# Kernel optimization log

Hardware: AMD Instinct MI355X
Metric: run time of the kernel (lower is better)

## Reference

```python
import jax, jax.numpy as jnp
import numpy as np

V, D, H, L, FF, NA, NB, S, C, BS = 32000, 768, 12, 6, 3072, 2, 2, 512, 10, 16
MOE_LAYERS = (1, 3, 5)
NE = NA * NB


def _ln(x, g, b, eps=1e-5):
    m = x.mean(-1, keepdims=True)
    v = ((x - m) ** 2).mean(-1, keepdims=True)
    return (x - m) / jnp.sqrt(v + eps) * g + b


def _ffn(x, W1, B1, W2, B2):
    # GLU-style FFN: w2(a * silu(b)) where [a, b] = chunk(w1(x), 2)
    h = x @ W1.T + B1
    a, b = jnp.split(h, 2, -1)
    return (a * jax.nn.silu(b)) @ W2.T + B2


def _mha(x, wqkv, bqkv, wo, bo):
    Bq, Sq, d = x.shape
    dh = d // H
    qkv = x @ wqkv.T + bqkv
    q, k, v = jnp.split(qkv, 3, -1)
    q = q.reshape(Bq, Sq, H, dh).transpose(0, 2, 1, 3)
    k = k.reshape(Bq, Sq, H, dh).transpose(0, 2, 1, 3)
    v = v.reshape(Bq, Sq, H, dh).transpose(0, 2, 1, 3)
    scores = jnp.einsum('bhqd,bhkd->bhqk', q, k) / jnp.sqrt(jnp.float32(dh))
    attn = jax.nn.softmax(scores, axis=-1)
    o = jnp.einsum('bhqk,bhkd->bhqd', attn, v)
    o = o.transpose(0, 2, 1, 3).reshape(Bq, Sq, d)
    return o @ wo.T + bo


def _moe(xf, W1, B1, W2, B2, gAw, gAb, gBw, gBb):
    pA = jax.nn.softmax(xf @ gAw.T + gAb, axis=-1)  # [T, NA]
    pB = jax.nn.softmax(xf @ gBw.T + gBb, axis=-1)  # [T, NB]
    iA = jnp.argmax(pA, -1)
    iB = jnp.argmax(pB, -1)
    auxA = NA * (pA.mean(0) * jax.nn.one_hot(iA, NA).mean(0)).sum()
    auxB = NB * (pB.mean(0) * jax.nn.one_hot(iB, NB).mean(0)).sum()
    e = iA * NB + iB  # [T] flattened expert id
    # dense all-expert compute then per-token select (E is small = 4)
    h = jnp.einsum('td,efd->etf', xf, W1) + B1[:, None, :]  # [NE, T, 2*FF]
    a, b = jnp.split(h, 2, -1)
    y = jnp.einsum('etf,edf->etd', a * jax.nn.silu(b), W2) + B2[:, None, :]
    out = y[e, jnp.arange(xf.shape[0])]  # [T, D]
    return out, auxA + auxB


def _forward(tok_emb, pos_emb, wqkv, bqkv, wo, bo, ln1g, ln1b, ln2g, ln2b,
             dW1, dB1, dW2, dB2, mW1, mB1, mW2, mB2, gAw, gAb, gBw, gBb,
             cW1, cB1, cW2, cB2, input_ids):
    x = tok_emb[input_ids] + pos_emb[None, :, :]
    total_aux = jnp.float32(0.0)
    di = mi = 0
    for l in range(L):
        x = _ln(x + _mha(x, wqkv[l], bqkv[l], wo[l], bo[l]), ln1g[l], ln1b[l])
        if l in MOE_LAYERS:
            xf = x.reshape(BS * S, D)
            f, aux = _moe(xf, mW1[mi], mB1[mi], mW2[mi], mB2[mi],
                          gAw[mi], gAb[mi], gBw[mi], gBb[mi])
            mi += 1
            total_aux = total_aux + aux
            f = f.reshape(BS, S, D)
        else:
            f = _ffn(x, dW1[di], dB1[di], dW2[di], dB2[di])
            di += 1
        x = _ln(x + f, ln2g[l], ln2b[l])
    rep = x.mean(1)  # mean pooling (no cls token / mask)
    hcls = jax.nn.relu(rep @ cW1.T + cB1)
    logits = hcls @ cW2.T + cB2
    return logits, total_aux


def setup_inputs() -> dict:
    key = jax.random.key(0)
    ks = iter(jax.random.split(key, 48))
    r = lambda shape, s=0.02: jax.random.normal(next(ks), shape, jnp.float32) * s
    Ld, Lm = L - len(MOE_LAYERS), len(MOE_LAYERS)
    return dict(
        input_ids=jax.random.randint(next(ks), (BS, S), 0, V),
        tok_emb=r((V, D)),
        pos_emb=r((S, D), 0.01),
        wqkv=r((L, 3 * D, D)), bqkv=jnp.zeros((L, 3 * D), jnp.float32),
        wo=r((L, D, D)), bo=jnp.zeros((L, D), jnp.float32),
        ln1g=jnp.ones((L, D), jnp.float32), ln1b=jnp.zeros((L, D), jnp.float32),
        ln2g=jnp.ones((L, D), jnp.float32), ln2b=jnp.zeros((L, D), jnp.float32),
        dW1=r((Ld, 2 * FF, D)), dB1=jnp.zeros((Ld, 2 * FF), jnp.float32),
        dW2=r((Ld, D, FF)), dB2=jnp.zeros((Ld, D), jnp.float32),
        mW1=r((Lm, NE, 2 * FF, D)), mB1=jnp.zeros((Lm, NE, 2 * FF), jnp.float32),
        mW2=r((Lm, NE, D, FF)), mB2=jnp.zeros((Lm, NE, D), jnp.float32),
        gAw=r((Lm, NA, D)), gAb=jnp.zeros((Lm, NA), jnp.float32),
        gBw=r((Lm, NB, D)), gBb=jnp.zeros((Lm, NB), jnp.float32),
        cW1=r((D, D)), cB1=jnp.zeros((D,), jnp.float32),
        cW2=r((C, D)), cB2=jnp.zeros((C,), jnp.float32),
    )


def reference(input_ids, tok_emb, pos_emb, wqkv, bqkv, wo, bo, ln1g, ln1b,
              ln2g, ln2b, dW1, dB1, dW2, dB2, mW1, mB1, mW2, mB2,
              gAw, gAb, gBw, gBb, cW1, cB1, cW2, cB2):
    return _forward(tok_emb, pos_emb, wqkv, bqkv, wo, bo, ln1g, ln1b, ln2g,
                    ln2b, dW1, dB1, dW2, dB2, mW1, mB1, mW2, mB2,
                    gAw, gAb, gBw, gBb, cW1, cB1, cW2, cB2, input_ids)
```

## Files before the change

### kernel.cpp

```cpp
#include <hip/hip_runtime.h>
#include <cstddef>

#define TOK   8192
#define DIMD  768
#define NH    12
#define DHD   64
#define SEQ   512
#define NB_   16
#define FFD   3072
#define NEXP  4
#define CCLS  10
#define FF2   (2*FFD)

typedef short bf16x8 __attribute__((ext_vector_type(8)));
typedef float f32x4  __attribute__((ext_vector_type(4)));

static const size_t OFF_X    = 0;
static const size_t OFF_XB   = OFF_X   + (size_t)TOK*DIMD;
static const size_t OFF_F    = OFF_XB  + (size_t)TOK*DIMD/2;
static const size_t OFF_SH   = OFF_F   + (size_t)TOK*DIMD;
static const size_t SH_FL    = (size_t)8704*FF2/2;
static const size_t OFF_WQ   = OFF_SH  + SH_FL;
static const size_t OFF_WOB  = OFF_WQ  + (size_t)3*DIMD*DIMD/2;
static const size_t OFF_W1B  = OFF_WOB + (size_t)DIMD*DIMD/2;
static const size_t OFF_W2B  = OFF_W1B + (size_t)NEXP*FF2*DIMD/2;
static const size_t OFF_REP  = OFF_W2B + (size_t)NEXP*DIMD*FFD/2;
static const size_t OFF_HCLS = OFF_REP + (size_t)NB_*DIMD;
static const size_t OFF_STAT = OFF_HCLS+ (size_t)NB_*DIMD;
static const size_t OFF_INT  = OFF_STAT+ 8;
static const size_t OFF_AUX  = OFF_INT + 160;
static const size_t OFF_EID  = OFF_AUX + 1;
static const size_t OFF_PERM = OFF_EID + TOK;

__device__ __forceinline__ ushort f2bf(float f) {
    union { float f; unsigned u; } v; v.f = f;
    unsigned r = v.u + 0x7FFF + ((v.u >> 16) & 1);
    return (ushort)(r >> 16);
}
__device__ __forceinline__ float bf2f(ushort u) {
    union { unsigned u; float f; } v; v.u = ((unsigned)u) << 16;
    return v.f;
}
__device__ __forceinline__ void gload16(const void* g, void* l) {
    __builtin_amdgcn_global_load_lds((const __attribute__((address_space(1))) void*)g,
                                     (__attribute__((address_space(3))) void*)l, 16, 0, 0);
}

__device__ __forceinline__ void xcd_swizzle_cm(int& bx, int& by)
{
    int gx = gridDim.x, gy = gridDim.y;
    int bid = blockIdx.x * gy + blockIdx.y;
    int nwg = gx * gy;
    int q = nwg >> 3, r8 = nwg & 7;
    int xcd = bid & 7, loc = bid >> 3;
    int lbid = (xcd < r8 ? xcd * (q + 1) : r8 * (q + 1) + (xcd - r8) * q) + loc;
    bx = lbid / gy;
    by = lbid % gy;
}

__global__ __launch_bounds__(256) void k_cvt(const float* __restrict__ s, ushort* __restrict__ d, int n8)
{
    int i = blockIdx.x * 256 + threadIdx.x;
    if (i >= n8) return;
    float4 x0 = ((const float4*)s)[i * 2];
    float4 x1 = ((const float4*)s)[i * 2 + 1];
    ushort r[8] = { f2bf(x0.x), f2bf(x0.y), f2bf(x0.z), f2bf(x0.w),
                    f2bf(x1.x), f2bf(x1.y), f2bf(x1.z), f2bf(x1.w) };
    ((uint4*)d)[i] = *(uint4*)r;
}

__global__ __launch_bounds__(256) void k_embed(const int* __restrict__ ids,
                                               const float* __restrict__ te,
                                               const float* __restrict__ pe,
                                               float* __restrict__ x,
                                               ushort* __restrict__ xb)
{
    int i = blockIdx.x * 256 + threadIdx.x;
    const int nd4 = DIMD / 4;
    if (i >= TOK * nd4) return;
    int t = i / nd4, d4 = i % nd4;
    int s = t % SEQ;
    int id = ids[t];
    float4 a = ((const float4*)(te + (size_t)id * DIMD))[d4];
    float4 b = ((const float4*)(pe + (size_t)s  * DIMD))[d4];
    float4 o; o.x = a.x + b.x; o.y = a.y + b.y; o.z = a.z + b.z; o.w = a.w + b.w;
    ((float4*)(x + (size_t)t * DIMD))[d4] = o;
    ushort4 ob = make_ushort4(f2bf(o.x), f2bf(o.y), f2bf(o.z), f2bf(o.w));
    *(ushort4*)(xb + (size_t)t * DIMD + d4 * 4) = ob;
}

template<int GATHER, int SCAT>
__global__ __launch_bounds__(256) void k_mm(const ushort* __restrict__ A,
                                            const ushort* __restrict__ Wb,
                                            const float* __restrict__ bias,
                                            ushort* __restrict__ C_,
                                            int N, int K, int lda,
                                            const int* __restrict__ perm,
                                            const int* __restrict__ offs,
                                            const int* __restrict__ blke,
                                            const int* __restrict__ blkb,
                                            const int* __restrict__ nblk)
{
    constexpr int MOE = GATHER || SCAT;
    __shared__ ushort As[2][4096];
    __shared__ ushort Bs[2][4096];
    __shared__ int    toks[128];
    const int tid = threadIdx.x, lane = tid & 63, w = tid >> 6;
    int bx, by;
    xcd_swizzle_cm(bx, by);
    const int n0 = bx * 128, row0 = by * 128;
    const ushort* W = Wb;
    const float*  bi = bias;
    int lb = 0, cnt = 1 << 30;
    if constexpr (MOE) {
        if (by >= *nblk) return;
        int e = blke[by];
        lb = blkb[by];
        int base = offs[e];
        cnt = offs[e + 1] - base;
        W  += (size_t)e * N * K;
        bi += (size_t)e * N;
        if (tid < 128) { int rg = lb + tid; toks[tid] = perm[base + (rg < cnt ? rg : cnt - 1)]; }
        __syncthreads();
    }
    int ar0, ar1;
    if constexpr (GATHER) { ar0 = toks[lane]; ar1 = toks[64 + lane]; }
    else                  { ar0 = row0 + lane; ar1 = row0 + 64 + lane; }
    const ushort* ap0 = A + (size_t)ar0 * lda + w * 8;
    const ushort* ap1 = A + (size_t)ar1 * lda + w * 8;
    const ushort* bp0 = W + (size_t)(n0 + lane) * K + w * 8;
    const ushort* bp1 = W + (size_t)(n0 + 64 + lane) * K + w * 8;

    const int l15 = lane & 15, l4 = lane >> 4;
    const int wm = w >> 1, wn = w & 1;
    f32x4 acc[4][4] = {};

    gload16(ap0, &As[0][w * 1024]);
    gload16(ap1, &As[0][w * 1024 + 512]);
    gload16(bp0, &Bs[0][w * 1024]);
    gload16(bp1, &Bs[0][w * 1024 + 512]);
    __syncthreads();

    const int NT = K / 32;
    int cur = 0;
    for (int t = 0; t < NT; ++t) {
        if (t + 1 < NT) {
            int ko = (t + 1) * 32;
            gload16(ap0 + ko, &As[cur ^ 1][w * 1024]);
            gload16(ap1 + ko, &As[cur ^ 1][w * 1024 + 512]);
            gload16(bp0 + ko, &Bs[cur ^ 1][w * 1024]);
            gload16(bp1 + ko, &Bs[cur ^ 1][w * 1024 + 512]);
        }
        bf16x8 af[4], bf_[4];
#pragma unroll
        for (int i = 0; i < 4; ++i) {
            af[i]  = *(const bf16x8*)&As[cur][l4 * 1024 + (wm * 64 + i * 16 + l15) * 8];
            bf_[i] = *(const bf16x8*)&Bs[cur][l4 * 1024 + (wn * 64 + i * 16 + l15) * 8];
        }
#pragma unroll
        for (int mi = 0; mi < 4; ++mi)
#pragma unroll
            for (int ni = 0; ni < 4; ++ni)
                acc[mi][ni] = __builtin_amdgcn_mfma_f32_16x16x32_bf16(af[mi], bf_[ni], acc[mi][ni], 0, 0, 0);
        __syncthreads();
        cur ^= 1;
    }
#pragma unroll
    for (int ni = 0; ni < 4; ++ni) {
        int col = n0 + wn * 64 + ni * 16 + l15;
        float bb = bi[col];
#pragma unroll
        for (int mi = 0; mi < 4; ++mi) {
            int ri = wm * 64 + mi * 16 + l4 * 4;
#pragma unroll
            for (int r = 0; r < 4; ++r) {
                float o = acc[mi][ni][r] + bb;
                if constexpr (SCAT) {
                    if (lb + ri + r < cnt)
                        C_[(size_t)toks[ri + r] * N + col] = f2bf(o);
                } else {
                    C_[(size_t)(row0 + ri + r) * N + col] = f2bf(o);
                }
            }
        }
    }
}

template<int MOE>
__global__ __launch_bounds__(256) void k_w1g(const ushort* __restrict__ A,
                                             const ushort* __restrict__ Wb,
                                             const float* __restrict__ bias,
                                             ushort* __restrict__ G,
                                             const int* __restrict__ perm,
                                             const int* __restrict__ offs,
                                             const int* __restrict__ blke,
                                             const int* __restrict__ blkb,
                                             const int* __restrict__ nblk)
{
    __shared__ ushort As[2][4096];
    __shared__ ushort Bs[2][8192];
    __shared__ int    toks[128];
    const int tid = threadIdx.x, lane = tid & 63, w = tid >> 6;
    int bx, by;
    xcd_swizzle_cm(bx, by);
    const int n0 = bx * 128, row0 = by * 128;
    const ushort* W = Wb;
    const float*  bi = bias;
    if constexpr (MOE) {
        if (by >= *nblk) return;
        int e = blke[by];
        W  += (size_t)e * FF2 * DIMD;
        bi += (size_t)e * FF2;
        int base = offs[e], cnt = offs[e + 1] - base, lb = blkb[by];
        if (tid < 128) { int rg = lb + tid; toks[tid] = perm[base + (rg < cnt ? rg : cnt - 1)]; }
        __syncthreads();
    }
    int ar0, ar1;
    if constexpr (MOE) { ar0 = toks[lane]; ar1 = toks[64 + lane]; }
    else               { ar0 = row0 + lane; ar1 = row0 + 64 + lane; }
    const ushort* ap0  = A + (size_t)ar0 * DIMD + w * 8;
    const ushort* ap1  = A + (size_t)ar1 * DIMD + w * 8;
    const ushort* bpa0 = W + (size_t)(n0 + lane) * DIMD + w * 8;
    const ushort* bpa1 = W + (size_t)(n0 + 64 + lane) * DIMD + w * 8;
    const ushort* bpb0 = W + (size_t)(FFD + n0 + lane) * DIMD + w * 8;
    const ushort* bpb1 = W + (size_t)(FFD + n0 + 64 + lane) * DIMD + w * 8;

    const int l15 = lane & 15, l4 = lane >> 4;
    const int wm = w >> 1, wn = w & 1;
    f32x4 accA[4][4] = {}, accB[4][4] = {};

    gload16(ap0,  &As[0][w * 1024]);
    gload16(ap1,  &As[0][w * 1024 + 512]);
    gload16(bpa0, &Bs[0][w * 2048]);
    gload16(bpa1, &Bs[0][w * 2048 + 512]);
    gload16(bpb0, &Bs[0][w * 2048 + 1024]);
    gload16(bpb1, &Bs[0][w * 2048 + 1536]);
    __syncthreads();

    const int NT = DIMD / 32;
    int cur = 0;
    for (int t = 0; t < NT; ++t) {
        if (t + 1 < NT) {
            int ko = (t + 1) * 32;
            gload16(ap0 + ko,  &As[cur ^ 1][w * 1024]);
            gload16(ap1 + ko,  &As[cur ^ 1][w * 1024 + 512]);
            gload16(bpa0 + ko, &Bs[cur ^ 1][w * 2048]);
            gload16(bpa1 + ko, &Bs[cur ^ 1][w * 2048 + 512]);
            gload16(bpb0 + ko, &Bs[cur ^ 1][w * 2048 + 1024]);
            gload16(bpb1 + ko, &Bs[cur ^ 1][w * 2048 + 1536]);
        }
        bf16x8 af[4], ba[4], bb[4];
#pragma unroll
        for (int i = 0; i < 4; ++i) {
            af[i] = *(const bf16x8*)&As[cur][l4 * 1024 + (wm * 64 + i * 16 + l15) * 8];
            ba[i] = *(const bf16x8*)&Bs[cur][l4 * 2048 + (wn * 64 + i * 16 + l15) * 8];
            bb[i] = *(const bf16x8*)&Bs[cur][l4 * 2048 + 1024 + (wn * 64 + i * 16 + l15) * 8];
        }
#pragma unroll
        for (int mi = 0; mi < 4; ++mi)
#pragma unroll
            for (int ni = 0; ni < 4; ++ni) {
                accA[mi][ni] = __builtin_amdgcn_mfma_f32_16x16x32_bf16(af[mi], ba[ni], accA[mi][ni], 0, 0, 0);
                accB[mi][ni] = __builtin_amdgcn_mfma_f32_16x16x32_bf16(af[mi], bb[ni], accB[mi][ni], 0, 0, 0);
            }
        __syncthreads();
        cur ^= 1;
    }
#pragma unroll
    for (int ni = 0; ni < 4; ++ni) {
        int col = n0 + wn * 64 + ni * 16 + l15;
        float fa = bi[col];
        float fb = bi[FFD + col];
#pragma unroll
        for (int mi = 0; mi < 4; ++mi) {
            int ri = wm * 64 + mi * 16 + l4 * 4;
#pragma unroll
            for (int r = 0; r < 4; ++r) {
                float a = accA[mi][ni][r] + fa;
                float b = accB[mi][ni][r] + fb;
                float g = a * (b / (1.f + __expf(-b)));
                G[(size_t)(row0 + ri + r) * FFD + col] = f2bf(g);
            }
        }
    }
}

__global__ __launch_bounds__(256) void k_attn(const ushort* __restrict__ qkv, ushort* __restrict__ out)
{
    __shared__ ushort Qs[64][72];
    __shared__ ushort Ks[64][72];
    __shared__ ushort Vt[64][72];
    __shared__ ushort Ps[4][16][72];
    const int bh = blockIdx.x;
    const int b = bh / NH, h = bh % NH;
    const int qt = blockIdx.y;
    const int tid = threadIdx.x, lane = tid & 63, w = tid >> 6;
    const int l15 = lane & 15, l4 = lane >> 4;
    const int t0 = b * SEQ + qt * 64;
    {
        int r = tid >> 3, c8 = (tid & 7) * 8;
#pragma unroll
        for (int p = 0; p < 2; ++p) {
            int rr = r + p * 32;
            *(uint4*)&Qs[rr][c8] = *(const uint4*)(qkv + (size_t)(t0 + rr) * 3 * DIMD + h * DHD + c8);
        }
    }
    __syncthreads();
    bf16x8 aq[2];
    aq[0] = *(const bf16x8*)&Qs[w*16 + l15][l4*8];
    aq[1] = *(const bf16x8*)&Qs[w*16 + l15][32 + l4*8];
    f32x4 o[4] = {};
    float m[4], lsum[4];
#pragma unroll
    for (int r = 0; r < 4; ++r) { m[r] = -3.0e38f; lsum[r] = 0.f; }
    for (int kt = 0; kt < SEQ; kt += 64) {
        __syncthreads();
        {
            int r = tid >> 3, c8 = (tid & 7) * 8;
#pragma unroll
            for (int p = 0; p < 2; ++p) {
                int rr = r + p * 32;
                const ushort* kp = qkv + (size_t)(b * SEQ + kt + rr) * 3 * DIMD + DIMD + h * DHD;
                *(uint4*)&Ks[rr][c8] = *(const uint4*)(kp + c8);
                uint4 vv = *(const uint4*)(kp + DIMD + c8);
                const ushort* vs = (const ushort*)&vv;
#pragma unroll
                for (int j = 0; j < 8; ++j) Vt[c8 + j][rr] = vs[j];
            }
        }
        __syncthreads();
        f32x4 s[4] = {};
#pragma unroll
        for (int kk = 0; kk < 2; ++kk)
#pragma unroll
            for (int ni = 0; ni < 4; ++ni) {
                bf16x8 bk = *(const bf16x8*)&Ks[ni*16 + l15][kk*32 + l4*8];
                s[ni] = __builtin_amdgcn_mfma_f32_16x16x32_bf16(aq[kk], bk, s[ni], 0, 0, 0);
            }
        float csc[4];
#pragma unroll
        for (int r = 0; r < 4; ++r) {
            float mx = -3.0e38f;
#pragma unroll
            for (int ni = 0; ni < 4; ++ni) { s[ni][r] *= 0.125f; mx = fmaxf(mx, s[ni][r]); }
            mx = fmaxf(mx, __shfl_xor(mx, 1));
            mx = fmaxf(mx, __shfl_xor(mx, 2));
            mx = fmaxf(mx, __shfl_xor(mx, 4));
            mx = fmaxf(mx, __shfl_xor(mx, 8));
            float nm = fmaxf(m[r], mx);
            float c = __expf(m[r] - nm);
            m[r] = nm;
            float ps = 0.f;
#pragma unroll
            for (int ni = 0; ni < 4; ++ni) { s[ni][r] = __expf(s[ni][r] - nm); ps += s[ni][r]; }
            ps += __shfl_xor(ps, 1);
            ps += __shfl_xor(ps, 2);
            ps += __shfl_xor(ps, 4);
            ps += __shfl_xor(ps, 8);
            lsum[r] = lsum[r] * c + ps;
            csc[r] = c;
#pragma unroll
            for (int ni = 0; ni < 4; ++ni)
                Ps[w][l4*4 + r][ni*16 + l15] = f2bf(s[ni][r]);
        }
#pragma unroll
        for (int di = 0; di < 4; ++di)
#pragma unroll
            for (int r = 0; r < 4; ++r) o[di][r] *= csc[r];
        bf16x8 ap[2];
        ap[0] = *(const bf16x8*)&Ps[w][l15][l4*8];
        ap[1] = *(const bf16x8*)&Ps[w][l15][32 + l4*8];
#pragma unroll
        for (int kk = 0; kk < 2; ++kk)
#pragma unroll
            for (int di = 0; di < 4; ++di) {
                bf16x8 bv = *(const bf16x8*)&Vt[di*16 + l15][kk*32 + l4*8];
                o[di] = __builtin_amdgcn_mfma_f32_16x16x32_bf16(ap[kk], bv, o[di], 0, 0, 0);
            }
    }
    float inv[4];
#pragma unroll
    for (int r = 0; r < 4; ++r) inv[r] = 1.f / lsum[r];
#pragma unroll
    for (int di = 0; di < 4; ++di)
#pragma unroll
        for (int r = 0; r < 4; ++r)
            out[(size_t)(t0 + w*16 + l4*4 + r) * DIMD + h * DHD + di*16 + l15] = f2bf(o[di][r] * inv[r]);
}

__global__ __launch_bounds__(256) void k_ln(float* __restrict__ x, const ushort* __restrict__ fb,
                                            const float* __restrict__ g, const float* __restrict__ b,
                                            ushort* __restrict__ xb)
{
    const int t = blockIdx.x * 4 + (threadIdx.x >> 6);
    const int lane = threadIdx.x & 63;
    float* xr = x + (size_t)t * DIMD;
    const ushort* fr = fb + (size_t)t * DIMD;
    float v[12];
    float s = 0.f, s2 = 0.f;
#pragma unroll
    for (int j = 0; j < 12; ++j) {
        int d = lane + j * 64;
        float val = xr[d] + bf2f(fr[d]);
        v[j] = val; s += val; s2 = fmaf(val, val, s2);
    }
#pragma unroll
    for (int off = 1; off < 64; off <<= 1) {
        s  += __shfl_xor(s,  off);
        s2 += __shfl_xor(s2, off);
    }
    const float mean = s * (1.f / DIMD);
    const float var  = s2 * (1.f / DIMD) - mean * mean;
    const float rstd = rsqrtf(var + 1e-5f);
#pragma unroll
    for (int j = 0; j < 12; ++j) {
        int d = lane + j * 64;
        float o = (v[j] - mean) * rstd * g[d] + b[d];
        xr[d] = o;
        xb[(size_t)t * DIMD + d] = f2bf(o);
    }
}

__global__ __launch_bounds__(256) void k_gate(const float* __restrict__ x,
                                              const float* __restrict__ gAw, const float* __restrict__ gAb,
                                              const float* __restrict__ gBw, const float* __restrict__ gBb,
                                              float* __restrict__ sums, int* __restrict__ cnts,
                                              int* __restrict__ e_id)
{
    const int tid = threadIdx.x, lane = tid & 63, wid = tid >> 6;
    const int gw = blockIdx.x * 4 + wid;
    float wA0[12], wA1[12], wB0[12], wB1[12];
#pragma unroll
    for (int i = 0; i < 12; ++i) {
        int d = lane + i * 64;
        wA0[i] = gAw[d]; wA1[i] = gAw[DIMD + d];
        wB0[i] = gBw[d]; wB1[i] = gBw[DIMD + d];
    }
    const float bA0 = gAb[0], bA1 = gAb[1], bB0 = gBb[0], bB1 = gBb[1];
    float sA0 = 0.f, sA1 = 0.f, sB0 = 0.f, sB1 = 0.f;
    int cA1 = 0, cB1 = 0, cE0 = 0, cE1 = 0, cE2 = 0;
    for (int i = 0; i < 32; ++i) {
        int t = gw * 32 + i;
        const float* xr = x + (size_t)t * DIMD;
        float a0 = 0.f, a1 = 0.f, b0 = 0.f, b1 = 0.f;
#pragma unroll
        for (int j = 0; j < 12; ++j) {
            float v = xr[lane + j * 64];
            a0 = fmaf(v, wA0[j], a0); a1 = fmaf(v, wA1[j], a1);
            b0 = fmaf(v, wB0[j], b0); b1 = fmaf(v, wB1[j], b1);
        }
#pragma unroll
        for (int off = 1; off < 64; off <<= 1) {
            a0 += __shfl_xor(a0, off); a1 += __shfl_xor(a1, off);
            b0 += __shfl_xor(b0, off); b1 += __shfl_xor(b1, off);
        }
        a0 += bA0; a1 += bA1; b0 += bB0; b1 += bB1;
        int iA = (a1 > a0) ? 1 : 0;
        int iB = (b1 > b0) ? 1 : 0;
        float mA = fmaxf(a0, a1); float eA0 = __expf(a0 - mA), eA1 = __expf(a1 - mA);
        float dA = 1.f / (eA0 + eA1);
        float mB = fmaxf(b0, b1); float eB0 = __expf(b0 - mB), eB1 = __expf(b1 - mB);
        float dB = 1.f / (eB0 + eB1);
        sA0 += eA0 * dA; sA1 += eA1 * dA;
        sB0 += eB0 * dB; sB1 += eB1 * dB;
        cA1 += iA; cB1 += iB;
        int e = iA * 2 + iB;
        cE0 += (e == 0); cE1 += (e == 1); cE2 += (e == 2);
        if (lane == 0) e_id[t] = e;
    }
    __shared__ float fpart[4][4];
    __shared__ int   ipart[4][8];
    if (lane == 0) {
        fpart[wid][0] = sA0; fpart[wid][1] = sA1; fpart[wid][2] = sB0; fpart[wid][3] = sB1;
        ipart[wid][0] = 32 - cA1; ipart[wid][1] = cA1;
        ipart[wid][2] = 32 - cB1; ipart[wid][3] = cB1;
        ipart[wid][4] = cE0; ipart[wid][5] = cE1; ipart[wid][6] = cE2;
        ipart[wid][7] = 32 - cE0 - cE1 - cE2;
    }
    __syncthreads();
    if (tid < 4)  atomicAdd(sums + tid, fpart[0][tid] + fpart[1][tid] + fpart[2][tid] + fpart[3][tid]);
    else if (tid >= 64 && tid < 72) {
        int k = tid - 64;
        atomicAdd(cnts + k, ipart[0][k] + ipart[1][k] + ipart[2][k] + ipart[3][k]);
    }
}

__global__ void k_offsets(const int* __restrict__ cntE, int* __restrict__ offs, int* __restrict__ cursor,
                          int* __restrict__ nblk, int* __restrict__ blke, int* __restrict__ blkb)
{
    if (threadIdx.x == 0) {
        int a = 0, nb = 0;
        for (int e = 0; e < NEXP; ++e) {
            offs[e] = a; a += cntE[e]; cursor[e] = 0;
            int blocks = (cntE[e] + 127) >> 7;
            for (int b = 0; b < blocks; ++b) { blke[nb] = e; blkb[nb] = b * 128; ++nb; }
        }
        offs[NEXP] = a;
        *nblk = nb;
    }
}

__global__ __launch_bounds__(256) void k_scatter(const int* __restrict__ e_id, const int* __restrict__ offs,
                                                 int* __restrict__ cursor, int* __restrict__ perm)
{
    int t = blockIdx.x * 256 + threadIdx.x;
    int lane = threadIdx.x & 63;
    int e = e_id[t];
#pragma unroll
    for (int eo = 0; eo < NEXP; ++eo) {
        unsigned long long m = __ballot(e == eo);
        if (m == 0ULL) continue;
        int leader = __ffsll((long long)m) - 1;
        int base = 0;
        if (lane == leader) base = atomicAdd(cursor + eo, (int)__popcll(m));
        base = __shfl(base, leader);
        if (e == eo) {
            int lower = (int)__popcll(m & ((1ULL << lane) - 1ULL));
            perm[offs[eo] + base + lower] = t;
        }
    }
}

__global__ void k_aux(const float* __restrict__ sums, const int* __restrict__ cnts, float* __restrict__ aux_acc)
{
    if (threadIdx.x == 0) {
        const float invT2 = 1.f / ((float)TOK * (float)TOK);
        float aA = 2.f * (sums[0] * (float)cnts[0] + sums[1] * (float)cnts[1]) * invT2;
        float aB = 2.f * (sums[2] * (float)cnts[2] + sums[3] * (float)cnts[3]) * invT2;
        *aux_acc += aA + aB;
    }
}

__global__ __launch_bounds__(256) void k_rep(const float* __restrict__ x, float* __restrict__ rep)
{
    int i = blockIdx.x * 256 + threadIdx.x;
    if (i >= NB_ * DIMD) return;
    int b = i / DIMD, d = i % DIMD;
    float s = 0.f;
    for (int q = 0; q < SEQ; ++q) s += x[((size_t)b * SEQ + q) * DIMD + d];
    rep[i] = s * (1.f / SEQ);
}

__global__ __launch_bounds__(256) void k_cls1(const float* __restrict__ rep, const float* __restrict__ cW1,
                                              const float* __restrict__ cB1, float* __restrict__ hcls)
{
    int w = blockIdx.x * 4 + (threadIdx.x >> 6);
    int lane = threadIdx.x & 63;
    if (w >= NB_ * DIMD) return;
    int b = w / DIMD, i = w % DIMD;
    float s = 0.f;
    for (int d = lane; d < DIMD; d += 64) s += rep[b * DIMD + d] * cW1[(size_t)i * DIMD + d];
    for (int off = 32; off > 0; off >>= 1) s += __shfl_down(s, off);
    if (lane == 0) hcls[w] = fmaxf(s + cB1[i], 0.f);
}

__global__ __launch_bounds__(256) void k_cls2(const float* __restrict__ hcls, const float* __restrict__ cW2,
                                              const float* __restrict__ cB2, float* __restrict__ out)
{
    int w = blockIdx.x * 4 + (threadIdx.x >> 6);
    int lane = threadIdx.x & 63;
    if (w >= NB_ * CCLS) return;
    int b = w / CCLS, c = w % CCLS;
    float s = 0.f;
    for (int d = lane; d < DIMD; d += 64) s += hcls[b * DIMD + d] * cW2[(size_t)c * DIMD + d];
    for (int off = 32; off > 0; off >>= 1) s += __shfl_down(s, off);
    if (lane == 0) out[w] = s + cB2[c];
}

__global__ void k_writeaux(const float* __restrict__ aux_acc, float* __restrict__ out)
{
    if (threadIdx.x == 0) out[NB_ * CCLS] = *aux_acc;
}

extern "C" void kernel_launch(void* const* d_in, const int* in_sizes, int n_in,
                              void* d_out, int out_size, void* d_ws, size_t ws_size,
                              hipStream_t stream)
{
    const int*   input_ids = (const int*)  d_in[0];
    const float* tok_emb   = (const float*)d_in[1];
    const float* pos_emb   = (const float*)d_in[2];
    const float* wqkv      = (const float*)d_in[3];
    const float* bqkv      = (const float*)d_in[4];
    const float* wo        = (const float*)d_in[5];
    const float* bo        = (const float*)d_in[6];
    const float* ln1g      = (const float*)d_in[7];
    const float* ln1b      = (const float*)d_in[8];
    const float* ln2g      = (const float*)d_in[9];
    const float* ln2b      = (const float*)d_in[10];
    const float* dW1       = (const float*)d_in[11];
    const float* dB1       = (const float*)d_in[12];
    const float* dW2       = (const float*)d_in[13];
    const float* dB2       = (const float*)d_in[14];
    const float* mW1       = (const float*)d_in[15];
    const float* mB1       = (const float*)d_in[16];
    const float* mW2       = (const float*)d_in[17];
    const float* mB2       = (const float*)d_in[18];
    const float* gAw       = (const float*)d_in[19];
    const float* gAb       = (const float*)d_in[20];
    const float* gBw       = (const float*)d_in[21];
    const float* gBb       = (const float*)d_in[22];
    const float* cW1       = (const float*)d_in[23];
    const float* cB1       = (const float*)d_in[24];
    const float* cW2       = (const float*)d_in[25];
    const float* cB2       = (const float*)d_in[26];

    float* out = (float*)d_out;
    float* ws  = (float*)d_ws;

    float*  X    = ws + OFF_X;
    ushort* XB   = (ushort*)(ws + OFF_XB);
    ushort* FB   = (ushort*)(ws + OFF_F);
    ushort* QKV  = (ushort*)(ws + OFF_SH);
    ushort* G    = (ushort*)(ws + OFF_SH + (size_t)TOK * 3 * DIMD / 2);
    ushort* Gg   = (ushort*)(ws + OFF_SH);
    ushort* WQB  = (ushort*)(ws + OFF_WQ);
    ushort* WOB  = (ushort*)(ws + OFF_WOB);
    ushort* W1B  = (ushort*)(ws + OFF_W1B);
    ushort* W2B  = (ushort*)(ws + OFF_W2B);
    float*  REP  = ws + OFF_REP;
    float*  HCLS = ws + OFF_HCLS;
    float*  SUMS = ws + OFF_STAT;
    int*    INTB = (int*)(ws + OFF_INT);
    int*    CNTS = INTB;
    int*    OFFS = INTB + 8;
    int*    CURS = INTB + 13;
    int*    NBLK = INTB + 17;
    int*    BLKE = INTB + 18;
    int*    BLKB = INTB + 86;
    float*  AUXP = ws + OFF_AUX;
    int*    EID  = (int*)(ws + OFF_EID);
    int*    PERM = (int*)(ws + OFF_PERM);

    hipMemsetAsync(AUXP, 0, sizeof(float), stream);

    k_embed<<<dim3((TOK * DIMD / 4) / 256), 256, 0, stream>>>(input_ids, tok_emb, pos_emb, X, XB);

    int di = 0, mi = 0;
    for (int l = 0; l < 6; ++l) {
        const int moe = (l == 1 || l == 3 || l == 5);
        {
            int n8 = 3 * DIMD * DIMD / 8;
            k_cvt<<<dim3((n8 + 255) / 256), 256, 0, stream>>>(wqkv + (size_t)l * 3 * DIMD * DIMD, WQB, n8);
            n8 = DIMD * DIMD / 8;
            k_cvt<<<dim3((n8 + 255) / 256), 256, 0, stream>>>(wo + (size_t)l * DIMD * DIMD, WOB, n8);
            if (moe) {
                n8 = NEXP * FF2 * DIMD / 8;
                k_cvt<<<dim3((n8 + 255) / 256), 256, 0, stream>>>(mW1 + (size_t)mi * NEXP * FF2 * DIMD, W1B, n8);
                n8 = NEXP * DIMD * FFD / 8;
                k_cvt<<<dim3((n8 + 255) / 256), 256, 0, stream>>>(mW2 + (size_t)mi * NEXP * DIMD * FFD, W2B, n8);
            } else {
                n8 = FF2 * DIMD / 8;
                k_cvt<<<dim3((n8 + 255) / 256), 256, 0, stream>>>(dW1 + (size_t)di * FF2 * DIMD, W1B, n8);
                n8 = DIMD * FFD / 8;
                k_cvt<<<dim3((n8 + 255) / 256), 256, 0, stream>>>(dW2 + (size_t)di * DIMD * FFD, W2B, n8);
            }
        }
        k_mm<0,0><<<dim3(3 * DIMD / 128, TOK / 128), 256, 0, stream>>>(
            XB, WQB, bqkv + (size_t)l * 3 * DIMD, QKV, 3 * DIMD, DIMD, DIMD,
            nullptr, nullptr, nullptr, nullptr, nullptr);
        k_attn<<<dim3(NB_ * NH, SEQ / 64), 256, 0, stream>>>(QKV, G);
        k_mm<0,0><<<dim3(DIMD / 128, TOK / 128), 256, 0, stream>>>(
            G, WOB, bo + (size_t)l * DIMD, FB, DIMD, DIMD, DIMD,
            nullptr, nullptr, nullptr, nullptr, nullptr);
        k_ln<<<TOK / 4, 256, 0, stream>>>(X, FB, ln1g + (size_t)l * DIMD, ln1b + (size_t)l * DIMD, XB);

        if (moe) {
            hipMemsetAsync(SUMS, 0, 64, stream);
            k_gate<<<64, 256, 0, stream>>>(X,
                gAw + (size_t)mi * 2 * DIMD, gAb + (size_t)mi * 2,
                gBw + (size_t)mi * 2 * DIMD, gBb + (size_t)mi * 2,
                SUMS, CNTS, EID);
            k_offsets<<<1, 1, 0, stream>>>(CNTS + 4, OFFS, CURS, NBLK, BLKE, BLKB);
            k_scatter<<<TOK / 256, 256, 0, stream>>>(EID, OFFS, CURS, PERM);
            k_w1g<1><<<dim3(FFD / 128, 68), 256, 0, stream>>>(
                XB, W1B, mB1 + (size_t)mi * NEXP * FF2, Gg,
                PERM, OFFS, BLKE, BLKB, NBLK);
            k_mm<0,1><<<dim3(DIMD / 128, 68), 256, 0, stream>>>(
                Gg, W2B, mB2 + (size_t)mi * NEXP * DIMD, FB, DIMD, FFD, FFD,
                PERM, OFFS, BLKE, BLKB, NBLK);
            k_aux<<<1, 1, 0, stream>>>(SUMS, CNTS, AUXP);
            ++mi;
        } else {
            k_w1g<0><<<dim3(FFD / 128, TOK / 128), 256, 0, stream>>>(
                XB, W1B, dB1 + (size_t)di * FF2, Gg,
                nullptr, nullptr, nullptr, nullptr, nullptr);
            k_mm<0,0><<<dim3(DIMD / 128, TOK / 128), 256, 0, stream>>>(
                Gg, W2B, dB2 + (size_t)di * DIMD, FB, DIMD, FFD, FFD,
                nullptr, nullptr, nullptr, nullptr, nullptr);
            ++di;
        }
        k_ln<<<TOK / 4, 256, 0, stream>>>(X, FB, ln2g + (size_t)l * DIMD, ln2b + (size_t)l * DIMD, XB);
    }

    k_rep<<<dim3((NB_ * DIMD + 255) / 256), 256, 0, stream>>>(X, REP);
    k_cls1<<<dim3(NB_ * DIMD / 4), 256, 0, stream>>>(REP, cW1, cB1, HCLS);
    k_cls2<<<dim3((NB_ * CCLS + 3) / 4), 256, 0, stream>>>(HCLS, cW2, cB2, out);
    k_writeaux<<<1, 1, 0, stream>>>(AUXP, out);
}
```

Before: 2.976 ms.

## Write QKV projection into head-major K and transposed V layouts for attention

Adds a dedicated QKV GEMM kernel whose epilogue writes Q row-major, K in per-head [S,dh] layout and V pre-transposed per head [dh,S]. The attention kernel then loads K and V tiles with contiguous 16-byte loads instead of strided row reads and an element-by-element scalar transpose of V into shared memory. The cost moves to the GEMM epilogue, whose V stores are scattered 2-byte writes with a large stride and may coalesce poorly.

After: 3.062 ms. 2.9% more time.

```diff
diff --git a/kernel.cpp b/kernel.cpp
--- a/kernel.cpp
+++ b/kernel.cpp
@@ -186,6 +186,86 @@
     }
 }
 
+__global__ __launch_bounds__(256) void k_qkv(const ushort* __restrict__ A,
+                                             const ushort* __restrict__ Wb,
+                                             const float* __restrict__ bias,
+                                             ushort* __restrict__ Qb,
+                                             ushort* __restrict__ Kb,
+                                             ushort* __restrict__ Vb)
+{
+    const int N = 3 * DIMD, K = DIMD;
+    __shared__ ushort As[2][4096];
+    __shared__ ushort Bs[2][4096];
+    const int tid = threadIdx.x, lane = tid & 63, w = tid >> 6;
+    int bx, by;
+    xcd_swizzle_cm(bx, by);
+    const int n0 = bx * 128, row0 = by * 128;
+    const ushort* ap0 = A + (size_t)(row0 + lane) * K + w * 8;
+    const ushort* ap1 = A + (size_t)(row0 + 64 + lane) * K + w * 8;
+    const ushort* bp0 = Wb + (size_t)(n0 + lane) * K + w * 8;
+    const ushort* bp1 = Wb + (size_t)(n0 + 64 + lane) * K + w * 8;
+
+    const int l15 = lane & 15, l4 = lane >> 4;
+    const int wm = w >> 1, wn = w & 1;
+    f32x4 acc[4][4] = {};
+
+    gload16(ap0, &As[0][w * 1024]);
+    gload16(ap1, &As[0][w * 1024 + 512]);
+    gload16(bp0, &Bs[0][w * 1024]);
+    gload16(bp1, &Bs[0][w * 1024 + 512]);
+    __syncthreads();
+
+    const int NT = K / 32;
+    int cur = 0;
+    for (int t = 0; t < NT; ++t) {
+        if (t + 1 < NT) {
+            int ko = (t + 1) * 32;
+            gload16(ap0 + ko, &As[cur ^ 1][w * 1024]);
+            gload16(ap1 + ko, &As[cur ^ 1][w * 1024 + 512]);
+            gload16(bp0 + ko, &Bs[cur ^ 1][w * 1024]);
+            gload16(bp1 + ko, &Bs[cur ^ 1][w * 1024 + 512]);
+        }
+        bf16x8 af[4], bf_[4];
+#pragma unroll
+        for (int i = 0; i < 4; ++i) {
+            af[i]  = *(const bf16x8*)&As[cur][l4 * 1024 + (wm * 64 + i * 16 + l15) * 8];
+            bf_[i] = *(const bf16x8*)&Bs[cur][l4 * 1024 + (wn * 64 + i * 16 + l15) * 8];
+        }
+#pragma unroll
+        for (int mi = 0; mi < 4; ++mi)
+#pragma unroll
+            for (int ni = 0; ni < 4; ++ni)
+                acc[mi][ni] = __builtin_amdgcn_mfma_f32_16x16x32_bf16(af[mi], bf_[ni], acc[mi][ni], 0, 0, 0);
+        __syncthreads();
+        cur ^= 1;
+    }
+#pragma unroll
+    for (int ni = 0; ni < 4; ++ni) {
+        int col = n0 + wn * 64 + ni * 16 + l15;
+        float bb = bias[col];
+#pragma unroll
+        for (int mi = 0; mi < 4; ++mi) {
+            int ri = wm * 64 + mi * 16 + l4 * 4;
+#pragma unroll
+            for (int r = 0; r < 4; ++r) {
+                float o = acc[mi][ni][r] + bb;
+                ushort v = f2bf(o);
+                int row = row0 + ri + r;
+                int bq = row >> 9, sq = row & 511;
+                if (col < DIMD) {
+                    Qb[(size_t)row * DIMD + col] = v;
+                } else if (col < 2 * DIMD) {
+                    int hh = (col - DIMD) >> 6, dd = (col - DIMD) & 63;
+                    Kb[(((size_t)(bq * NH + hh)) * SEQ + sq) * DHD + dd] = v;
+                } else {
+                    int hh = (col - 2 * DIMD) >> 6, dd = (col - 2 * DIMD) & 63;
+                    Vb[(((size_t)(bq * NH + hh)) * DHD + dd) * SEQ + sq] = v;
+                }
+            }
+        }
+    }
+}
+
 template<int MOE>
 __global__ __launch_bounds__(256) void k_w1g(const ushort* __restrict__ A,
                                              const ushort* __restrict__ Wb,
@@ -285,7 +365,10 @@
     }
 }
 
-__global__ __launch_bounds__(256) void k_attn(const ushort* __restrict__ qkv, ushort* __restrict__ out)
+__global__ __launch_bounds__(256) void k_attn(const ushort* __restrict__ Qb,
+                                              const ushort* __restrict__ Kb,
+                                              const ushort* __restrict__ Vb,
+                                              ushort* __restrict__ out)
 {
     __shared__ ushort Qs[64][72];
     __shared__ ushort Ks[64][72];
@@ -297,12 +380,14 @@
     const int tid = threadIdx.x, lane = tid & 63, w = tid >> 6;
     const int l15 = lane & 15, l4 = lane >> 4;
     const int t0 = b * SEQ + qt * 64;
+    const ushort* kbase = Kb + (size_t)bh * SEQ * DHD;
+    const ushort* vbase = Vb + (size_t)bh * DHD * SEQ;
     {
         int r = tid >> 3, c8 = (tid & 7) * 8;
 #pragma unroll
         for (int p = 0; p < 2; ++p) {
             int rr = r + p * 32;
-            *(uint4*)&Qs[rr][c8] = *(const uint4*)(qkv + (size_t)(t0 + rr) * 3 * DIMD + h * DHD + c8);
+            *(uint4*)&Qs[rr][c8] = *(const uint4*)(Qb + (size_t)(t0 + rr) * DIMD + h * DHD + c8);
         }
     }
     __syncthreads();
@@ -320,13 +405,11 @@
 #pragma unroll
             for (int p = 0; p < 2; ++p) {
                 int rr = r + p * 32;
-                const ushort* kp = qkv + (size_t)(b * SEQ + kt + rr) * 3 * DIMD + DIMD + h * DHD;
-                *(uint4*)&Ks[rr][c8] = *(const uint4*)(kp + c8);
-                uint4 vv = *(const uint4*)(kp + DIMD + c8);
-                const ushort* vs = (const ushort*)&vv;
-#pragma unroll
-                for (int j = 0; j < 8; ++j) Vt[c8 + j][rr] = vs[j];
+                *(uint4*)&Ks[rr][c8] = *(const uint4*)(kbase + (size_t)(kt + rr) * DHD + c8);
             }
+            int d = tid >> 2, c8v = (tid & 3) * 8;
+            *(uint4*)&Vt[d][c8v]      = *(const uint4*)(vbase + (size_t)d * SEQ + kt + c8v);
+            *(uint4*)&Vt[d][32 + c8v] = *(const uint4*)(vbase + (size_t)d * SEQ + kt + 32 + c8v);
         }
         __syncthreads();
         f32x4 s[4] = {};
@@ -610,7 +693,9 @@
     float*  X    = ws + OFF_X;
     ushort* XB   = (ushort*)(ws + OFF_XB);
     ushort* FB   = (ushort*)(ws + OFF_F);
-    ushort* QKV  = (ushort*)(ws + OFF_SH);
+    ushort* Qb   = (ushort*)(ws + OFF_SH);
+    ushort* Kb   = Qb + (size_t)TOK * DIMD;
+    ushort* Vb   = Kb + (size_t)TOK * DIMD;
     ushort* G    = (ushort*)(ws + OFF_SH + (size_t)TOK * 3 * DIMD / 2);
     ushort* Gg   = (ushort*)(ws + OFF_SH);
     ushort* WQB  = (ushort*)(ws + OFF_WQ);
@@ -655,10 +740,9 @@
                 k_cvt<<<dim3((n8 + 255) / 256), 256, 0, stream>>>(dW2 + (size_t)di * DIMD * FFD, W2B, n8);
             }
         }
-        k_mm<0,0><<<dim3(3 * DIMD / 128, TOK / 128), 256, 0, stream>>>(
-            XB, WQB, bqkv + (size_t)l * 3 * DIMD, QKV, 3 * DIMD, DIMD, DIMD,
-            nullptr, nullptr, nullptr, nullptr, nullptr);
-        k_attn<<<dim3(NB_ * NH, SEQ / 64), 256, 0, stream>>>(QKV, G);
+        k_qkv<<<dim3(3 * DIMD / 128, TOK / 128), 256, 0, stream>>>(
+            XB, WQB, bqkv + (size_t)l * 3 * DIMD, Qb, Kb, Vb);
+        k_attn<<<dim3(NB_ * NH, SEQ / 64), 256, 0, stream>>>(Qb, Kb, Vb, G);
         k_mm<0,0><<<dim3(DIMD / 128, TOK / 128), 256, 0, stream>>>(
             G, WOB, bo + (size_t)l * DIMD, FB, DIMD, DIMD, DIMD,
             nullptr, nullptr, nullptr, nullptr, nullptr);
```
